# Kernel tuning notes

Hardware: AMD Instinct MI355X
Metric: run time of the kernel (lower is better)

The kernel has to match this reference:

```python
import jax, jax.numpy as jnp
import numpy as np

EPS = 1e-5

def _bn(x, g, b, axes):
    m = jnp.mean(x, axes, keepdims=True)
    v = jnp.var(x, axes, keepdims=True)
    return (x - m) * jax.lax.rsqrt(v + EPS) * g + b

def _fps(p, m):
    # farthest point sampling: p [B,N,3] -> int32 indices [B,m]
    B, N, _ = p.shape
    def step(carry, _):
        mind, last = carry
        lastp = jnp.take_along_axis(p, last[:, None, None], axis=1)[:, 0]  # [B,3]
        d = jnp.sum((p - lastp[:, None, :]) ** 2, axis=-1)                 # [B,N]
        mind = jnp.minimum(mind, d)
        nxt = jnp.argmax(mind, axis=1).astype(jnp.int32)
        return (mind, nxt), last
    init = (jnp.full((B, N), jnp.inf, p.dtype), jnp.zeros((B,), jnp.int32))
    _, idxs = jax.lax.scan(step, init, None, length=m)  # [m,B]
    return idxs.T

def _gather(x, idx):
    # x [B,N,C], idx [B,...] -> [B,...,C]
    B, C = x.shape[0], x.shape[-1]
    flat = idx.reshape(B, -1)
    out = jnp.take_along_axis(x, flat[:, :, None], axis=1)
    return out.reshape(idx.shape + (C,))

def _transition_down(p, h, W, g, b, stride, nsample):
    # p [B,N,3], h [B,N,C] -> new_p [B,N//stride,3], y [B,N//stride,Cout]
    B, N, _ = p.shape
    M = N // stride
    idx = _fps(p, M)
    new_p = _gather(p, idx)                                               # [B,M,3]
    d = jnp.sum((new_p[:, :, None, :] - p[:, None, :, :]) ** 2, axis=-1)  # [B,M,N]
    _, nidx = jax.lax.top_k(-d, nsample)                                  # [B,M,k]
    gp = _gather(p, nidx) - new_p[:, :, None, :]                          # rel xyz [B,M,k,3]
    gx = _gather(h, nidx)                                                 # [B,M,k,C]
    feat = jnp.concatenate([gp, gx], axis=-1)                             # with_xyz=True
    y = jnp.einsum('bmkc,cd->bmkd', feat, W)
    y = jax.nn.relu(_bn(y, g, b, (0, 1, 2)))
    return new_p, jnp.max(y, axis=2)                                      # MaxPool1d(nsample)

def _forward(x, W1, g1, b1, W2, g2, b2, W3, g3, b3, W4, g4, b4, W5, g5, b5,
             Wc1, bc1, gc1, hc1, Wc2, bc2, gc2, hc2, Wc3, bc3):
    p = x[..., :3]                                    # in_channels == 3 -> features = xyz
    h = jnp.einsum('bnc,cd->bnd', p, W1)
    h = jax.nn.relu(_bn(h, g1, b1, (0, 1)))           # enc1: stride=1
    p, h = _transition_down(p, h, W2, g2, b2, 4, 16)  # enc2
    p, h = _transition_down(p, h, W3, g3, b3, 4, 16)  # enc3
    p, h = _transition_down(p, h, W4, g4, b4, 4, 16)  # enc4
    p, h = _transition_down(p, h, W5, g5, b5, 4, 16)  # enc5
    z = jnp.mean(h, axis=1)                           # segment-mean pool -> [B,512]
    z = jax.nn.relu(_bn(z @ Wc1 + bc1, gc1, hc1, (0,)))   # Dropout = identity (eval)
    z = jax.nn.relu(_bn(z @ Wc2 + bc2, gc2, hc2, (0,)))
    return z @ Wc3 + bc3                              # [B,40]

def setup_inputs() -> dict:
    key = jax.random.key(0)
    ks = jax.random.split(key, 16)
    B, N = 16, 4096
    def lin(k, fi, fo):
        return (jax.random.normal(k, (fi, fo), jnp.float32) / np.sqrt(fi)).astype(jnp.float32)
    inp = {"x": jax.random.normal(ks[0], (B, N, 3), jnp.float32)}
    planes = [32, 64, 128, 256, 512]
    ins = [3, 3 + 32, 3 + 64, 3 + 128, 3 + 256]
    for i, (fi, fo) in enumerate(zip(ins, planes), start=1):
        inp[f"W{i}"] = lin(ks[i], fi, fo)
        inp[f"g{i}"] = jnp.ones((fo,), jnp.float32)
        inp[f"b{i}"] = jnp.zeros((fo,), jnp.float32)
    dims = [(512, 256), (256, 128), (128, 40)]
    for j, (fi, fo) in enumerate(dims, start=1):
        inp[f"Wc{j}"] = lin(ks[5 + j], fi, fo)
        inp[f"bc{j}"] = jnp.zeros((fo,), jnp.float32)
        if j < 3:
            inp[f"gc{j}"] = jnp.ones((fo,), jnp.float32)
            inp[f"hc{j}"] = jnp.zeros((fo,), jnp.float32)
    return inp

def reference(x, W1, g1, b1, W2, g2, b2, W3, g3, b3, W4, g4, b4, W5, g5, b5,
              Wc1, bc1, gc1, hc1, Wc2, bc2, gc2, hc2, Wc3, bc3):
    return _forward(x, W1, g1, b1, W2, g2, b2, W3, g3, b3, W4, g4, b4, W5, g5, b5,
                    Wc1, bc1, gc1, hc1, Wc2, bc2, gc2, hc2, Wc3, bc3)
```

## Files before the change

### kernel.cpp

```cpp
#include <hip/hip_runtime.h>
#include <math.h>
#include <float.h>

#define BN_EPS 1e-5f

__device__ __forceinline__ float sqdist_exact(float dx, float dy, float dz) {
  return __fadd_rn(__fadd_rn(__fmul_rn(dx, dx), __fmul_rn(dy, dy)), __fmul_rn(dz, dz));
}

__global__ void __launch_bounds__(256) mlp1_kernel(const float* __restrict__ x,
                                                   const float* __restrict__ W1,
                                                   float* __restrict__ h1, int rows) {
  int tid = blockIdx.x * 256 + threadIdx.x;
  int row = tid >> 5;
  int d = tid & 31;
  if (row >= rows) return;
  float x0 = x[row * 3 + 0], x1 = x[row * 3 + 1], x2 = x[row * 3 + 2];
  float acc = x0 * W1[d] + x1 * W1[32 + d] + x2 * W1[64 + d];
  h1[row * 32 + d] = acc;
}

__global__ void stats_kernel(const float* __restrict__ v, int n, int D,
                             float* __restrict__ partial) {
  int tid = blockIdx.x * blockDim.x + threadIdx.x;
  int stride = blockDim.x * gridDim.x;
  float s = 0.f, q = 0.f;
  for (int i = tid; i < n; i += stride) { float a = v[i]; s += a; q += a * a; }
  int c = tid % D;
  extern __shared__ float sm[];
  for (int i = threadIdx.x; i < 2 * D; i += blockDim.x) sm[i] = 0.f;
  __syncthreads();
  atomicAdd(&sm[c], s);
  atomicAdd(&sm[D + c], q);
  __syncthreads();
  for (int i = threadIdx.x; i < 2 * D; i += blockDim.x)
    atomicAdd(&partial[(blockIdx.x & 63) * 2 * D + i], sm[i]);
}

__global__ void finalize_kernel(const float* __restrict__ partial,
                                const float* __restrict__ g, const float* __restrict__ b,
                                float cnt, int D, float* __restrict__ ss) {
  int d = threadIdx.x;
  if (d >= D) return;
  float s = 0.f, q = 0.f;
  for (int j = 0; j < 64; j++) { s += partial[j * 2 * D + d]; q += partial[j * 2 * D + D + d]; }
  float mean = s / cnt;
  float var = q / cnt - mean * mean;
  var = fmaxf(var, 0.f);
  float sc = g[d] * rsqrtf(var + BN_EPS);
  ss[d] = sc;
  ss[D + d] = b[d] - mean * sc;
}

__global__ void bn_apply_kernel(float* __restrict__ vmax, const float* __restrict__ vmin,
                                const float* __restrict__ ss, int D, int n) {
  int tid = blockIdx.x * blockDim.x + threadIdx.x;
  int stride = blockDim.x * gridDim.x;
  for (int i = tid; i < n; i += stride) {
    int d = i % D;
    float sc = ss[d], sh = ss[D + d];
    float v = (sc >= 0.f) ? vmax[i] : vmin[i];
    vmax[i] = fmaxf(v * sc + sh, 0.f);
  }
}

#define DPP_STEP(CTRL)                                                                   \
  {                                                                                      \
    unsigned int nhi = (unsigned int)__builtin_amdgcn_update_dpp((int)khi, (int)khi,     \
                                                                 CTRL, 0xf, 0xf, false); \
    unsigned int nlo = (unsigned int)__builtin_amdgcn_update_dpp((int)klo, (int)klo,     \
                                                                 CTRL, 0xf, 0xf, false); \
    unsigned long long nk = (((unsigned long long)nhi) << 32) | nlo;                     \
    if (nk > wk) { wk = nk; khi = nhi; klo = nlo; }                                      \
  }

template <int P, int NW>
__global__ void __launch_bounds__(NW * 64) fps4_kernel(const float* __restrict__ p,
                                                       float* __restrict__ newp) {
  constexpr int BS = NW * 64;
  constexpr int N = P * BS;
  constexpr int M = N / 4;
  __shared__ float spts[N * 3];
  __shared__ float snew[NW > 1 ? M * 3 : 1];
  __shared__ unsigned long long slots[NW > 1 ? 2 * NW : 2];
  const int b = blockIdx.x;
  const int t = threadIdx.x;
  const int wv = t >> 6;
  const int lane = t & 63;
  const float* pb = p + (size_t)b * N * 3;
  float px[P], py[P], pz[P], md[P];
#pragma unroll
  for (int j = 0; j < P; j++) {
    int i = j * BS + t;
    float x = pb[3 * i], y = pb[3 * i + 1], z = pb[3 * i + 2];
    px[j] = x; py[j] = y; pz[j] = z; md[j] = INFINITY;
    spts[3 * i] = x; spts[3 * i + 1] = y; spts[3 * i + 2] = z;
  }
  float lx = pb[0], ly = pb[1], lz = pb[2];
  if (t == 0) {
    if constexpr (NW > 1) {
      snew[0] = lx; snew[1] = ly; snew[2] = lz;
    } else {
      newp[(size_t)b * M * 3 + 0] = lx;
      newp[(size_t)b * M * 3 + 1] = ly;
      newp[(size_t)b * M * 3 + 2] = lz;
    }
  }

  for (int r = 1; r < M; r++) {
    float bv; int bi;
    {
      float d0 = sqdist_exact(px[0] - lx, py[0] - ly, pz[0] - lz);
      float m0 = fminf(md[0], d0);
      md[0] = m0;
      bv = m0; bi = t;
    }
#pragma unroll
    for (int j = 1; j < P; j++) {
      float d = sqdist_exact(px[j] - lx, py[j] - ly, pz[j] - lz);
      float m = fminf(md[j], d);
      md[j] = m;
      if (m > bv) { bv = m; bi = j * BS + t; }
    }
    unsigned int khi = __float_as_uint(bv);
    unsigned int klo = ~(unsigned int)bi;
    unsigned long long wk = (((unsigned long long)khi) << 32) | klo;
    DPP_STEP(0x111);
    DPP_STEP(0x112);
    DPP_STEP(0x114);
    DPP_STEP(0x118);
    DPP_STEP(0x142);
    DPP_STEP(0x143);
    unsigned int gidx;
    if constexpr (NW == 1) {
      unsigned int wlo = (unsigned int)__builtin_amdgcn_readlane((int)wk, 63);
      gidx = ~wlo;
    } else {
      unsigned long long* base = slots + (r & 1) * NW;
      if (lane == 63) base[wv] = wk;
      __syncthreads();
      unsigned long long fk = base[0];
#pragma unroll
      for (int w = 1; w < NW; w++) {
        unsigned long long k2 = base[w];
        if (k2 > fk) fk = k2;
      }
      gidx = ~(unsigned int)fk;
    }
    lx = spts[3 * gidx];
    ly = spts[3 * gidx + 1];
    lz = spts[3 * gidx + 2];
    if (t == 0) {
      if constexpr (NW > 1) {
        snew[3 * r] = lx; snew[3 * r + 1] = ly; snew[3 * r + 2] = lz;
      } else {
        size_t o = ((size_t)b * M + r) * 3;
        newp[o] = lx; newp[o + 1] = ly; newp[o + 2] = lz;
      }
    }
  }
  if constexpr (NW > 1) {
    __syncthreads();
    for (int i = t; i < M * 3; i += BS) newp[(size_t)b * M * 3 + i] = snew[i];
  }
}

__global__ void __launch_bounds__(256) knn_kernel(const float* __restrict__ p,
                                                  const float* __restrict__ newp,
                                                  int N, int M, int BM,
                                                  int* __restrict__ nidx) {
  int gwid = (blockIdx.x * 256 + threadIdx.x) >> 6;
  int lane = threadIdx.x & 63;
  if (gwid >= BM) return;
  int b = gwid / M;
  const float* pb = p + (size_t)b * N * 3;
  float qx = newp[(size_t)gwid * 3], qy = newp[(size_t)gwid * 3 + 1], qz = newp[(size_t)gwid * 3 + 2];
  float bd[16];
  int bi[16];
#pragma unroll
  for (int s = 0; s < 16; s++) { bd[s] = INFINITY; bi[s] = 0x7FFFFFFF; }
  for (int c = lane; c < N; c += 64) {
    float d = sqdist_exact(pb[3 * c] - qx, pb[3 * c + 1] - qy, pb[3 * c + 2] - qz);
    if (d < bd[15]) {
      bd[15] = d; bi[15] = c;
#pragma unroll
      for (int s = 15; s >= 1; --s) {
        bool sw = bd[s] < bd[s - 1];
        if (sw) {
          float tf = bd[s]; bd[s] = bd[s - 1]; bd[s - 1] = tf;
          int ti = bi[s]; bi[s] = bi[s - 1]; bi[s - 1] = ti;
        }
      }
    }
  }
  int out = 0;
  for (int r = 0; r < 16; r++) {
    float v = bd[0]; int ii = bi[0];
    float mv = v; int mi = ii;
#pragma unroll
    for (int m = 1; m < 64; m <<= 1) {
      float v2 = __shfl_xor(mv, m);
      int i2 = __shfl_xor(mi, m);
      if (v2 < mv || (v2 == mv && i2 < mi)) { mv = v2; mi = i2; }
    }
    if (mi == ii) {
#pragma unroll
      for (int s = 0; s < 15; s++) { bd[s] = bd[s + 1]; bi[s] = bi[s + 1]; }
      bd[15] = INFINITY; bi[15] = 0x7FFFFFFF;
    }
    if (lane == r) out = mi;
  }
  if (lane < 16) nidx[(size_t)gwid * 16 + lane] = out;
}

__global__ void __launch_bounds__(256) gemm_kernel(
    const float* __restrict__ p, const float* __restrict__ h, const float* __restrict__ newp,
    const int* __restrict__ nidx, const float* __restrict__ W,
    float* __restrict__ ymax, float* __restrict__ ymin, float* __restrict__ partial,
    int N, int M, int BM, int Ch, int Cpad, int D, int Gseq) {
  extern __shared__ float sm[];
  int Ctot = Ch + 3;
  int TD = D < 256 ? D : 256;
  int Gpar = 256 / TD;
  float* sfeat = sm;
  float* sstat = sm + Gpar * 16 * Cpad;
  int t = threadIdx.x;
  for (int i = t; i < 2 * D; i += 256) sstat[i] = 0.f;
  int mloc = t / TD;
  int dbase = t % TD;
  int DV = D / TD;
  __syncthreads();
  for (int s = 0; s < Gseq; s++) {
    int grp0 = (blockIdx.x * Gseq + s) * Gpar;
    if (grp0 >= BM) break;
    int nf = Gpar * 16 * Cpad;
    for (int i = t; i < nf; i += 256) {
      int c = i % Cpad;
      int rk = i / Cpad;
      int k = rk & 15;
      int g = rk >> 4;
      int grp = grp0 + g;
      float val = 0.f;
      if (grp < BM && c < Ctot) {
        int b = grp / M;
        int nb = nidx[(size_t)grp * 16 + k];
        if (c < 3)
          val = p[((size_t)b * N + nb) * 3 + c] - newp[(size_t)grp * 3 + c];
        else
          val = h[((size_t)b * N + nb) * Ch + (c - 3)];
      }
      sfeat[i] = val;
    }
    __syncthreads();
    int grp = grp0 + mloc;
    bool act = grp < BM;
    const float* fr = sfeat + mloc * 16 * Cpad;
    for (int dv = 0; dv < DV; ++dv) {
      int d = dbase + (dv << 8);
      float acc[16];
#pragma unroll
      for (int k = 0; k < 16; k++) acc[k] = 0.f;
      for (int c = 0; c < Cpad; c += 4) {
        float w0 = (c < Ctot) ? W[(size_t)c * D + d] : 0.f;
        float w1 = (c + 1 < Ctot) ? W[(size_t)(c + 1) * D + d] : 0.f;
        float w2 = (c + 2 < Ctot) ? W[(size_t)(c + 2) * D + d] : 0.f;
        float w3 = (c + 3 < Ctot) ? W[(size_t)(c + 3) * D + d] : 0.f;
#pragma unroll
        for (int k = 0; k < 16; k++) {
          const float4 f = *reinterpret_cast<const float4*>(fr + k * Cpad + c);
          acc[k] += f.x * w0 + f.y * w1 + f.z * w2 + f.w * w3;
        }
      }
      if (act) {
        float ssum = 0.f, ssq = 0.f, amax = -INFINITY, amin = INFINITY;
#pragma unroll
        for (int k = 0; k < 16; k++) {
          float a = acc[k];
          ssum += a; ssq += a * a;
          amax = fmaxf(amax, a); amin = fminf(amin, a);
        }
        ymax[(size_t)grp * D + d] = amax;
        ymin[(size_t)grp * D + d] = amin;
        atomicAdd(&sstat[d], ssum);
        atomicAdd(&sstat[D + d], ssq);
      }
    }
    __syncthreads();
  }
  for (int i = t; i < 2 * D; i += 256)
    atomicAdd(&partial[(blockIdx.x & 63) * 2 * D + i], sstat[i]);
}

__global__ void __launch_bounds__(512) classifier_kernel(
    const float* __restrict__ h4,
    const float* __restrict__ Wc1, const float* __restrict__ bc1,
    const float* __restrict__ gc1, const float* __restrict__ hc1,
    const float* __restrict__ Wc2, const float* __restrict__ bc2,
    const float* __restrict__ gc2, const float* __restrict__ hc2,
    const float* __restrict__ Wc3, const float* __restrict__ bc3,
    float* __restrict__ out) {
  __shared__ float z[16 * 512];
  __shared__ float z1[16 * 256];
  __shared__ float z2[16 * 128];
  __shared__ float sc[256], sh[256];
  int t = threadIdx.x;
  for (int i = t; i < 16 * 512; i += 512) {
    int b = i >> 9, c = i & 511;
    float s = 0.f;
    for (int k = 0; k < 16; k++) s += h4[((size_t)b * 16 + k) * 512 + c];
    z[i] = s * (1.f / 16.f);
  }
  __syncthreads();
  for (int i = t; i < 16 * 256; i += 512) {
    int b = i >> 8, d = i & 255;
    float a = bc1[d];
    for (int c = 0; c < 512; c++) a += z[(b << 9) + c] * Wc1[c * 256 + d];
    z1[i] = a;
  }
  __syncthreads();
  if (t < 256) {
    float s = 0.f, q = 0.f;
    for (int b = 0; b < 16; b++) { float a = z1[(b << 8) + t]; s += a; q += a * a; }
    float mean = s * (1.f / 16.f);
    float var = fmaxf(q * (1.f / 16.f) - mean * mean, 0.f);
    float scl = gc1[t] * rsqrtf(var + BN_EPS);
    sc[t] = scl; sh[t] = hc1[t] - mean * scl;
  }
  __syncthreads();
  for (int i = t; i < 16 * 256; i += 512) {
    int d = i & 255;
    z1[i] = fmaxf(z1[i] * sc[d] + sh[d], 0.f);
  }
  __syncthreads();
  for (int i = t; i < 16 * 128; i += 512) {
    int b = i >> 7, d = i & 127;
    float a = bc2[d];
    for (int c = 0; c < 256; c++) a += z1[(b << 8) + c] * Wc2[c * 128 + d];
    z2[i] = a;
  }
  __syncthreads();
  if (t < 128) {
    float s = 0.f, q = 0.f;
    for (int b = 0; b < 16; b++) { float a = z2[(b << 7) + t]; s += a; q += a * a; }
    float mean = s * (1.f / 16.f);
    float var = fmaxf(q * (1.f / 16.f) - mean * mean, 0.f);
    float scl = gc2[t] * rsqrtf(var + BN_EPS);
    sc[t] = scl; sh[t] = hc2[t] - mean * scl;
  }
  __syncthreads();
  for (int i = t; i < 16 * 128; i += 512) {
    int d = i & 127;
    z2[i] = fmaxf(z2[i] * sc[d] + sh[d], 0.f);
  }
  __syncthreads();
  for (int i = t; i < 640; i += 512) {
    int b = i / 40, d = i % 40;
    float a = bc3[d];
    for (int c = 0; c < 128; c++) a += z2[(b << 7) + c] * Wc3[c * 40 + d];
    out[i] = a;
  }
}

extern "C" void kernel_launch(void* const* d_in, const int* in_sizes, int n_in,
                              void* d_out, int out_size, void* d_ws, size_t ws_size,
                              hipStream_t stream) {
  (void)in_sizes; (void)n_in; (void)out_size; (void)ws_size;
  const float* x   = (const float*)d_in[0];
  const float* W1  = (const float*)d_in[1];
  const float* g1  = (const float*)d_in[2];
  const float* b1  = (const float*)d_in[3];
  const float* W2  = (const float*)d_in[4];
  const float* g2  = (const float*)d_in[5];
  const float* b2  = (const float*)d_in[6];
  const float* W3  = (const float*)d_in[7];
  const float* g3  = (const float*)d_in[8];
  const float* b3  = (const float*)d_in[9];
  const float* W4  = (const float*)d_in[10];
  const float* g4  = (const float*)d_in[11];
  const float* b4  = (const float*)d_in[12];
  const float* W5  = (const float*)d_in[13];
  const float* g5  = (const float*)d_in[14];
  const float* b5  = (const float*)d_in[15];
  const float* Wc1 = (const float*)d_in[16];
  const float* bc1 = (const float*)d_in[17];
  const float* gc1 = (const float*)d_in[18];
  const float* hc1 = (const float*)d_in[19];
  const float* Wc2 = (const float*)d_in[20];
  const float* bc2 = (const float*)d_in[21];
  const float* gc2 = (const float*)d_in[22];
  const float* hc2 = (const float*)d_in[23];
  const float* Wc3 = (const float*)d_in[24];
  const float* bc3 = (const float*)d_in[25];
  float* out = (float*)d_out;

  float* ws = (float*)d_ws;
  float* HA   = ws;
  float* HB   = HA + 2097152;
  float* YMIN = HB + 1048576;
  float* NP1  = YMIN + 1048576;
  float* NP2  = NP1 + 49152;
  float* NP3  = NP2 + 12288;
  float* NP4  = NP3 + 3072;
  int*   NIDX = (int*)(NP4 + 768);
  float* PART = (float*)(NIDX + 262144);
  float* SS   = PART + 5 * 65536;

  hipMemsetAsync(PART, 0, 5 * 65536 * sizeof(float), stream);

  mlp1_kernel<<<(65536 * 32) / 256, 256, 0, stream>>>(x, W1, HA, 65536);
  stats_kernel<<<256, 256, 2 * 32 * sizeof(float), stream>>>(HA, 65536 * 32, 32, PART);
  finalize_kernel<<<1, 32, 0, stream>>>(PART, g1, b1, 65536.f, 32, SS);
  bn_apply_kernel<<<512, 256, 0, stream>>>(HA, HA, SS, 32, 65536 * 32);

  fps4_kernel<16, 4><<<16, 256, 0, stream>>>(x, NP1);
  knn_kernel<<<(16384 + 3) / 4, 256, 0, stream>>>(x, NP1, 4096, 1024, 16384, NIDX);
  gemm_kernel<<<512, 256, (4 * 16 * 36 + 2 * 64) * sizeof(float), stream>>>(
      x, HA, NP1, NIDX, W2, HB, YMIN, PART + 65536, 4096, 1024, 16384, 32, 36, 64, 8);
  finalize_kernel<<<1, 64, 0, stream>>>(PART + 65536, g2, b2, (float)(16384 * 16), 64, SS + 1024);
  bn_apply_kernel<<<512, 256, 0, stream>>>(HB, YMIN, SS + 1024, 64, 16384 * 64);

  fps4_kernel<4, 4><<<16, 256, 0, stream>>>(NP1, NP2);
  knn_kernel<<<(4096 + 3) / 4, 256, 0, stream>>>(NP1, NP2, 1024, 256, 4096, NIDX);
  gemm_kernel<<<512, 256, (2 * 16 * 68 + 2 * 128) * sizeof(float), stream>>>(
      NP1, HB, NP2, NIDX, W3, HA, YMIN, PART + 2 * 65536, 1024, 256, 4096, 64, 68, 128, 4);
  finalize_kernel<<<1, 128, 0, stream>>>(PART + 2 * 65536, g3, b3, (float)(4096 * 16), 128, SS + 2048);
  bn_apply_kernel<<<512, 256, 0, stream>>>(HA, YMIN, SS + 2048, 128, 4096 * 128);

  fps4_kernel<4, 1><<<16, 64, 0, stream>>>(NP2, NP3);
  knn_kernel<<<(1024 + 3) / 4, 256, 0, stream>>>(NP2, NP3, 256, 64, 1024, NIDX);
  gemm_kernel<<<512, 256, (16 * 132 + 2 * 256) * sizeof(float), stream>>>(
      NP2, HA, NP3, NIDX, W4, HB, YMIN, PART + 3 * 65536, 256, 64, 1024, 128, 132, 256, 2);
  finalize_kernel<<<1, 256, 0, stream>>>(PART + 3 * 65536, g4, b4, (float)(1024 * 16), 256, SS + 3072);
  bn_apply_kernel<<<512, 256, 0, stream>>>(HB, YMIN, SS + 3072, 256, 1024 * 256);

  fps4_kernel<1, 1><<<16, 64, 0, stream>>>(NP3, NP4);
  knn_kernel<<<(256 + 3) / 4, 256, 0, stream>>>(NP3, NP4, 64, 16, 256, NIDX);
  gemm_kernel<<<256, 256, (16 * 260 + 2 * 512) * sizeof(float), stream>>>(
      NP3, HB, NP4, NIDX, W5, HA, YMIN, PART + 4 * 65536, 64, 16, 256, 256, 260, 512, 1);
  finalize_kernel<<<1, 512, 0, stream>>>(PART + 4 * 65536, g5, b5, (float)(256 * 16), 512, SS + 4096);
  bn_apply_kernel<<<512, 256, 0, stream>>>(HA, YMIN, SS + 4096, 512, 256 * 512);

  classifier_kernel<<<1, 512, 0, stream>>>(HA, Wc1, bc1, gc1, hc1, Wc2, bc2, gc2, hc2, Wc3, bc3, out);
}
```

Baseline: 1.524 ms.

## Carry winner coordinates through FPS reductions instead of shared-memory point lookup

The farthest-point-sampling kernel now carries the candidate's xyz along with its (distance, index) key through the per-thread tree reduction, the DPP wave reduction and the cross-wave shared slots. This removes the shared-memory copy of all points and the dependent LDS load of the winner's coordinates on each iteration's critical path. The per-thread argmax also becomes a pairwise tree instead of a linear chain, which shortens the dependency depth. In exchange each DPP step moves three extra registers and the per-thread selects handle more values, which adds ALU and register pressure.

```diff
diff --git a/kernel.cpp b/kernel.cpp
--- a/kernel.cpp
+++ b/kernel.cpp
@@ -70,8 +70,17 @@
                                                                  CTRL, 0xf, 0xf, false); \
     unsigned int nlo = (unsigned int)__builtin_amdgcn_update_dpp((int)klo, (int)klo,     \
                                                                  CTRL, 0xf, 0xf, false); \
+    int nxi = __builtin_amdgcn_update_dpp(__float_as_int(cx), __float_as_int(cx),        \
+                                          CTRL, 0xf, 0xf, false);                        \
+    int nyi = __builtin_amdgcn_update_dpp(__float_as_int(cy), __float_as_int(cy),        \
+                                          CTRL, 0xf, 0xf, false);                        \
+    int nzi = __builtin_amdgcn_update_dpp(__float_as_int(cz), __float_as_int(cz),        \
+                                          CTRL, 0xf, 0xf, false);                        \
     unsigned long long nk = (((unsigned long long)nhi) << 32) | nlo;                     \
-    if (nk > wk) { wk = nk; khi = nhi; klo = nlo; }                                      \
+    if (nk > wk) {                                                                       \
+      wk = nk; khi = nhi; klo = nlo;                                                     \
+      cx = __int_as_float(nxi); cy = __int_as_float(nyi); cz = __int_as_float(nzi);      \
+    }                                                                                    \
   }
 
 template <int P, int NW>
@@ -80,9 +89,9 @@
   constexpr int BS = NW * 64;
   constexpr int N = P * BS;
   constexpr int M = N / 4;
-  __shared__ float spts[N * 3];
   __shared__ float snew[NW > 1 ? M * 3 : 1];
-  __shared__ unsigned long long slots[NW > 1 ? 2 * NW : 2];
+  __shared__ unsigned long long skey[NW > 1 ? 2 * NW : 2];
+  __shared__ float scrd[NW > 1 ? 2 * NW * 3 : 6];
   const int b = blockIdx.x;
   const int t = threadIdx.x;
   const int wv = t >> 6;
@@ -92,9 +101,8 @@
 #pragma unroll
   for (int j = 0; j < P; j++) {
     int i = j * BS + t;
-    float x = pb[3 * i], y = pb[3 * i + 1], z = pb[3 * i + 2];
-    px[j] = x; py[j] = y; pz[j] = z; md[j] = INFINITY;
-    spts[3 * i] = x; spts[3 * i + 1] = y; spts[3 * i + 2] = z;
+    px[j] = pb[3 * i]; py[j] = pb[3 * i + 1]; pz[j] = pb[3 * i + 2];
+    md[j] = INFINITY;
   }
   float lx = pb[0], ly = pb[1], lz = pb[2];
   if (t == 0) {
@@ -108,22 +116,44 @@
   }
 
   for (int r = 1; r < M; r++) {
-    float bv; int bi;
-    {
-      float d0 = sqdist_exact(px[0] - lx, py[0] - ly, pz[0] - lz);
-      float m0 = fminf(md[0], d0);
-      md[0] = m0;
-      bv = m0; bi = t;
-    }
-#pragma unroll
-    for (int j = 1; j < P; j++) {
+#pragma unroll
+    for (int j = 0; j < P; j++) {
       float d = sqdist_exact(px[j] - lx, py[j] - ly, pz[j] - lz);
-      float m = fminf(md[j], d);
-      md[j] = m;
-      if (m > bv) { bv = m; bi = j * BS + t; }
+      md[j] = fminf(md[j], d);
+    }
+    float bv, cx, cy, cz;
+    unsigned int bi;
+    if constexpr (P == 1) {
+      bv = md[0]; bi = (unsigned int)t; cx = px[0]; cy = py[0]; cz = pz[0];
+    } else {
+      constexpr int H = P / 2;
+      float tv[H], tx[H], ty[H], tz[H];
+      unsigned int ti_[H];
+#pragma unroll
+      for (int j = 0; j < H; j++) {
+        bool tk = md[2 * j + 1] > md[2 * j];
+        tv[j] = tk ? md[2 * j + 1] : md[2 * j];
+        ti_[j] = tk ? (unsigned int)((2 * j + 1) * BS + t) : (unsigned int)(2 * j * BS + t);
+        tx[j] = tk ? px[2 * j + 1] : px[2 * j];
+        ty[j] = tk ? py[2 * j + 1] : py[2 * j];
+        tz[j] = tk ? pz[2 * j + 1] : pz[2 * j];
+      }
+#pragma unroll
+      for (int n = H; n > 1; n >>= 1) {
+#pragma unroll
+        for (int j = 0; j < n / 2; j++) {
+          bool tk = tv[2 * j + 1] > tv[2 * j];
+          tv[j] = tk ? tv[2 * j + 1] : tv[2 * j];
+          ti_[j] = tk ? ti_[2 * j + 1] : ti_[2 * j];
+          tx[j] = tk ? tx[2 * j + 1] : tx[2 * j];
+          ty[j] = tk ? ty[2 * j + 1] : ty[2 * j];
+          tz[j] = tk ? tz[2 * j + 1] : tz[2 * j];
+        }
+      }
+      bv = tv[0]; bi = ti_[0]; cx = tx[0]; cy = ty[0]; cz = tz[0];
     }
     unsigned int khi = __float_as_uint(bv);
-    unsigned int klo = ~(unsigned int)bi;
+    unsigned int klo = ~bi;
     unsigned long long wk = (((unsigned long long)khi) << 32) | klo;
     DPP_STEP(0x111);
     DPP_STEP(0x112);
@@ -131,25 +161,32 @@
     DPP_STEP(0x118);
     DPP_STEP(0x142);
     DPP_STEP(0x143);
-    unsigned int gidx;
     if constexpr (NW == 1) {
-      unsigned int wlo = (unsigned int)__builtin_amdgcn_readlane((int)wk, 63);
-      gidx = ~wlo;
+      lx = __int_as_float(__builtin_amdgcn_readlane(__float_as_int(cx), 63));
+      ly = __int_as_float(__builtin_amdgcn_readlane(__float_as_int(cy), 63));
+      lz = __int_as_float(__builtin_amdgcn_readlane(__float_as_int(cz), 63));
     } else {
-      unsigned long long* base = slots + (r & 1) * NW;
-      if (lane == 63) base[wv] = wk;
+      int base = (r & 1) * NW;
+      if (lane == 63) {
+        skey[base + wv] = wk;
+        scrd[(base + wv) * 3 + 0] = cx;
+        scrd[(base + wv) * 3 + 1] = cy;
+        scrd[(base + wv) * 3 + 2] = cz;
+      }
       __syncthreads();
-      unsigned long long fk = base[0];
+      unsigned long long fk = skey[base];
+      float fx = scrd[base * 3 + 0], fy = scrd[base * 3 + 1], fz = scrd[base * 3 + 2];
 #pragma unroll
       for (int w = 1; w < NW; w++) {
-        unsigned long long k2 = base[w];
-        if (k2 > fk) fk = k2;
-      }
-      gidx = ~(unsigned int)fk;
-    }
-    lx = spts[3 * gidx];
-    ly = spts[3 * gidx + 1];
-    lz = spts[3 * gidx + 2];
+        unsigned long long k2 = skey[base + w];
+        bool tk = k2 > fk;
+        fk = tk ? k2 : fk;
+        fx = tk ? scrd[(base + w) * 3 + 0] : fx;
+        fy = tk ? scrd[(base + w) * 3 + 1] : fy;
+        fz = tk ? scrd[(base + w) * 3 + 2] : fz;
+      }
+      lx = fx; ly = fy; lz = fz;
+    }
     if (t == 0) {
       if constexpr (NW > 1) {
         snew[3 * r] = lx; snew[3 * r + 1] = ly; snew[3 * r + 2] = lz;
```

Result: slower. 4.596 ms (+201.6%).

## Fuse next-stage FPS with current-stage KNN into one launch

Applied to the files above, without the earlier changes.

Factors FPS and KNN bodies into device functions and adds a fused kernel where the first 16 blocks run the next level's farthest point sampling while the remaining blocks run the current level's KNN. Since FPS depends only on coordinates, the serial FPS work can overlap with KNN and three launches are removed. The risk is the long-running FPS blocks sharing the GPU with KNN blocks and the larger 256-thread launch bound for single-wave FPS variants.

```diff
diff --git a/kernel.cpp b/kernel.cpp
--- a/kernel.cpp
+++ b/kernel.cpp
@@ -75,19 +75,15 @@
   }
 
 template <int P, int NW>
-__global__ void __launch_bounds__(NW * 64) fps4_kernel(const float* __restrict__ p,
-                                                       float* __restrict__ newp) {
+__device__ __forceinline__ void fps_body(const float* __restrict__ pb,
+                                         float* __restrict__ newp_b,
+                                         float* spts, float* snew,
+                                         unsigned long long* slots, int t) {
   constexpr int BS = NW * 64;
   constexpr int N = P * BS;
   constexpr int M = N / 4;
-  __shared__ float spts[N * 3];
-  __shared__ float snew[NW > 1 ? M * 3 : 1];
-  __shared__ unsigned long long slots[NW > 1 ? 2 * NW : 2];
-  const int b = blockIdx.x;
-  const int t = threadIdx.x;
   const int wv = t >> 6;
   const int lane = t & 63;
-  const float* pb = p + (size_t)b * N * 3;
   float px[P], py[P], pz[P], md[P];
 #pragma unroll
   for (int j = 0; j < P; j++) {
@@ -101,9 +97,7 @@
     if constexpr (NW > 1) {
       snew[0] = lx; snew[1] = ly; snew[2] = lz;
     } else {
-      newp[(size_t)b * M * 3 + 0] = lx;
-      newp[(size_t)b * M * 3 + 1] = ly;
-      newp[(size_t)b * M * 3 + 2] = lz;
+      newp_b[0] = lx; newp_b[1] = ly; newp_b[2] = lz;
     }
   }
 
@@ -154,15 +148,74 @@
       if constexpr (NW > 1) {
         snew[3 * r] = lx; snew[3 * r + 1] = ly; snew[3 * r + 2] = lz;
       } else {
-        size_t o = ((size_t)b * M + r) * 3;
-        newp[o] = lx; newp[o + 1] = ly; newp[o + 2] = lz;
+        newp_b[3 * r] = lx; newp_b[3 * r + 1] = ly; newp_b[3 * r + 2] = lz;
       }
     }
   }
   if constexpr (NW > 1) {
     __syncthreads();
-    for (int i = t; i < M * 3; i += BS) newp[(size_t)b * M * 3 + i] = snew[i];
-  }
+    for (int i = t; i < M * 3; i += BS) newp_b[i] = snew[i];
+  }
+}
+
+template <int P, int NW>
+__global__ void __launch_bounds__(NW * 64) fps4_kernel(const float* __restrict__ p,
+                                                       float* __restrict__ newp) {
+  constexpr int BS = NW * 64;
+  constexpr int N = P * BS;
+  constexpr int M = N / 4;
+  __shared__ float spts[N * 3];
+  __shared__ float snew[NW > 1 ? M * 3 : 1];
+  __shared__ unsigned long long slots[NW > 1 ? 2 * NW : 2];
+  fps_body<P, NW>(p + (size_t)blockIdx.x * N * 3, newp + (size_t)blockIdx.x * M * 3,
+                  spts, snew, slots, threadIdx.x);
+}
+
+__device__ __forceinline__ void knn_body(const float* __restrict__ p,
+                                         const float* __restrict__ newp,
+                                         int N, int M, int BM,
+                                         int* __restrict__ nidx,
+                                         int gwid, int lane) {
+  if (gwid >= BM) return;
+  int b = gwid / M;
+  const float* pb = p + (size_t)b * N * 3;
+  float qx = newp[(size_t)gwid * 3], qy = newp[(size_t)gwid * 3 + 1], qz = newp[(size_t)gwid * 3 + 2];
+  float bd[16];
+  int bi[16];
+#pragma unroll
+  for (int s = 0; s < 16; s++) { bd[s] = INFINITY; bi[s] = 0x7FFFFFFF; }
+  for (int c = lane; c < N; c += 64) {
+    float d = sqdist_exact(pb[3 * c] - qx, pb[3 * c + 1] - qy, pb[3 * c + 2] - qz);
+    if (d < bd[15]) {
+      bd[15] = d; bi[15] = c;
+#pragma unroll
+      for (int s = 15; s >= 1; --s) {
+        bool sw = bd[s] < bd[s - 1];
+        if (sw) {
+          float tf = bd[s]; bd[s] = bd[s - 1]; bd[s - 1] = tf;
+          int ti = bi[s]; bi[s] = bi[s - 1]; bi[s - 1] = ti;
+        }
+      }
+    }
+  }
+  int out = 0;
+  for (int r = 0; r < 16; r++) {
+    float v = bd[0]; int ii = bi[0];
+    float mv = v; int mi = ii;
+#pragma unroll
+    for (int m = 1; m < 64; m <<= 1) {
+      float v2 = __shfl_xor(mv, m);
+      int i2 = __shfl_xor(mi, m);
+      if (v2 < mv || (v2 == mv && i2 < mi)) { mv = v2; mi = i2; }
+    }
+    if (mi == ii) {
+#pragma unroll
+      for (int s = 0; s < 15; s++) { bd[s] = bd[s + 1]; bi[s] = bi[s + 1]; }
+      bd[15] = INFINITY; bi[15] = 0x7FFFFFFF;
+    }
+    if (lane == r) out = mi;
+  }
+  if (lane < 16) nidx[(size_t)gwid * 16 + lane] = out;
 }
 
 __global__ void __launch_bounds__(256) knn_kernel(const float* __restrict__ p,
@@ -171,46 +224,31 @@
                                                   int* __restrict__ nidx) {
   int gwid = (blockIdx.x * 256 + threadIdx.x) >> 6;
   int lane = threadIdx.x & 63;
-  if (gwid >= BM) return;
-  int b = gwid / M;
-  const float* pb = p + (size_t)b * N * 3;
-  float qx = newp[(size_t)gwid * 3], qy = newp[(size_t)gwid * 3 + 1], qz = newp[(size_t)gwid * 3 + 2];
-  float bd[16];
-  int bi[16];
-#pragma unroll
-  for (int s = 0; s < 16; s++) { bd[s] = INFINITY; bi[s] = 0x7FFFFFFF; }
-  for (int c = lane; c < N; c += 64) {
-    float d = sqdist_exact(pb[3 * c] - qx, pb[3 * c + 1] - qy, pb[3 * c + 2] - qz);
-    if (d < bd[15]) {
-      bd[15] = d; bi[15] = c;
-#pragma unroll
-      for (int s = 15; s >= 1; --s) {
-        bool sw = bd[s] < bd[s - 1];
-        if (sw) {
-          float tf = bd[s]; bd[s] = bd[s - 1]; bd[s - 1] = tf;
-          int ti = bi[s]; bi[s] = bi[s - 1]; bi[s - 1] = ti;
-        }
-      }
-    }
-  }
-  int out = 0;
-  for (int r = 0; r < 16; r++) {
-    float v = bd[0]; int ii = bi[0];
-    float mv = v; int mi = ii;
-#pragma unroll
-    for (int m = 1; m < 64; m <<= 1) {
-      float v2 = __shfl_xor(mv, m);
-      int i2 = __shfl_xor(mi, m);
-      if (v2 < mv || (v2 == mv && i2 < mi)) { mv = v2; mi = i2; }
-    }
-    if (mi == ii) {
-#pragma unroll
-      for (int s = 0; s < 15; s++) { bd[s] = bd[s + 1]; bi[s] = bi[s + 1]; }
-      bd[15] = INFINITY; bi[15] = 0x7FFFFFFF;
-    }
-    if (lane == r) out = mi;
-  }
-  if (lane < 16) nidx[(size_t)gwid * 16 + lane] = out;
+  knn_body(p, newp, N, M, BM, nidx, gwid, lane);
+}
+
+template <int P, int NW>
+__global__ void __launch_bounds__(256) fused_fps_knn_kernel(
+    const float* __restrict__ fp, float* __restrict__ fnewp,
+    const float* __restrict__ kp, const float* __restrict__ knewp,
+    int kN, int kM, int kBM, int* __restrict__ knidx) {
+  constexpr int BS = NW * 64;
+  constexpr int N = P * BS;
+  constexpr int M = N / 4;
+  __shared__ float spts[N * 3];
+  __shared__ float snew[NW > 1 ? M * 3 : 1];
+  __shared__ unsigned long long slots[NW > 1 ? 2 * NW : 2];
+  const int t = threadIdx.x;
+  if (blockIdx.x < 16) {
+    if (NW > 1 || t < 64) {
+      fps_body<P, NW>(fp + (size_t)blockIdx.x * N * 3, fnewp + (size_t)blockIdx.x * M * 3,
+                      spts, snew, slots, t);
+    }
+  } else {
+    int gwid = ((blockIdx.x - 16) * 256 + t) >> 6;
+    int lane = t & 63;
+    knn_body(kp, knewp, kN, kM, kBM, knidx, gwid, lane);
+  }
 }
 
 __global__ void __launch_bounds__(256) gemm_kernel(
@@ -413,27 +451,27 @@
   bn_apply_kernel<<<512, 256, 0, stream>>>(HA, HA, SS, 32, 65536 * 32);
 
   fps4_kernel<16, 4><<<16, 256, 0, stream>>>(x, NP1);
-  knn_kernel<<<(16384 + 3) / 4, 256, 0, stream>>>(x, NP1, 4096, 1024, 16384, NIDX);
+  fused_fps_knn_kernel<4, 4><<<16 + 4096, 256, 0, stream>>>(
+      NP1, NP2, x, NP1, 4096, 1024, 16384, NIDX);
   gemm_kernel<<<512, 256, (4 * 16 * 36 + 2 * 64) * sizeof(float), stream>>>(
       x, HA, NP1, NIDX, W2, HB, YMIN, PART + 65536, 4096, 1024, 16384, 32, 36, 64, 8);
   finalize_kernel<<<1, 64, 0, stream>>>(PART + 65536, g2, b2, (float)(16384 * 16), 64, SS + 1024);
   bn_apply_kernel<<<512, 256, 0, stream>>>(HB, YMIN, SS + 1024, 64, 16384 * 64);
 
-  fps4_kernel<4, 4><<<16, 256, 0, stream>>>(NP1, NP2);
-  knn_kernel<<<(4096 + 3) / 4, 256, 0, stream>>>(NP1, NP2, 1024, 256, 4096, NIDX);
+  fused_fps_knn_kernel<4, 1><<<16 + 1024, 256, 0, stream>>>(
+      NP2, NP3, NP1, NP2, 1024, 256, 4096, NIDX);
   gemm_kernel<<<512, 256, (2 * 16 * 68 + 2 * 128) * sizeof(float), stream>>>(
       NP1, HB, NP2, NIDX, W3, HA, YMIN, PART + 2 * 65536, 1024, 256, 4096, 64, 68, 128, 4);
   finalize_kernel<<<1, 128, 0, stream>>>(PART + 2 * 65536, g3, b3, (float)(4096 * 16), 128, SS + 2048);
   bn_apply_kernel<<<512, 256, 0, stream>>>(HA, YMIN, SS + 2048, 128, 4096 * 128);
 
-  fps4_kernel<4, 1><<<16, 64, 0, stream>>>(NP2, NP3);
-  knn_kernel<<<(1024 + 3) / 4, 256, 0, stream>>>(NP2, NP3, 256, 64, 1024, NIDX);
+  fused_fps_knn_kernel<1, 1><<<16 + 256, 256, 0, stream>>>(
+      NP3, NP4, NP2, NP3, 256, 64, 1024, NIDX);
   gemm_kernel<<<512, 256, (16 * 132 + 2 * 256) * sizeof(float), stream>>>(
       NP2, HA, NP3, NIDX, W4, HB, YMIN, PART + 3 * 65536, 256, 64, 1024, 128, 132, 256, 2);
   finalize_kernel<<<1, 256, 0, stream>>>(PART + 3 * 65536, g4, b4, (float)(1024 * 16), 256, SS + 3072);
   bn_apply_kernel<<<512, 256, 0, stream>>>(HB, YMIN, SS + 3072, 256, 1024 * 256);
 
-  fps4_kernel<1, 1><<<16, 64, 0, stream>>>(NP3, NP4);
   knn_kernel<<<(256 + 3) / 4, 256, 0, stream>>>(NP3, NP4, 64, 16, 256, NIDX);
   gemm_kernel<<<256, 256, (16 * 260 + 2 * 512) * sizeof(float), stream>>>(
       NP3, HB, NP4, NIDX, W5, HA, YMIN, PART + 4 * 65536, 64, 16, 256, 256, 260, 512, 1);
```

New measurement: 1.439 ms. 5.6% less time.
